# Kernel tuning notes

Hardware: AMD Instinct MI355X
Metric: run time of the kernel (lower is better)

Reference implementation:

```python
import jax, jax.numpy as jnp
import numpy as np

B, C, H, W, D = 512, 256, 6, 8, 8


def setup_inputs() -> dict:
    key = jax.random.key(0)
    k1, k2, k3 = jax.random.split(key, 3)
    x = jax.random.normal(k1, (B, C, H, W, D), dtype=jnp.float32)
    adj = jax.random.normal(k2, (C, C), dtype=jnp.float32)
    para = jax.random.normal(k3, (1, C, H, W, D), dtype=jnp.float32)
    return {"x": x, "adj": adj, "para": para}


def reference(x, adj, para):
    b, c, h, w, d = x.shape
    fea = x.reshape(b, c, h * w * d)              # (b, c, HWD)
    c_adj = x.mean(axis=(2, 3, 4))                # AdaptiveAvgPool3d(1) -> (b, c)
    # torch: t1 (1,c), t2 (c,1); (t1 - t2)[i, j] = c_adj[j] - c_adj[i]
    diff = c_adj[:, None, :] - c_adj[:, :, None]  # (b, c, c)
    s = jnp.abs(jnp.abs(jax.nn.sigmoid(diff) - 0.5) - 0.5) * 2.0
    s = (s + jnp.swapaxes(s, 1, 2)) * 0.5         # symmetrize
    # batched (adj * s) @ fea  -> (b, c, HWD)
    out = jnp.einsum('bij,bjk->bik', adj[None, :, :] * s, fea)
    out = out.reshape(b, c, h, w, d) * para       # broadcast (1,c,h,w,d)
    return jax.nn.relu(out)
```

## Files before the change

kernel.cpp:

```cpp
#include <hip/hip_runtime.h>

#define B_   512
#define C_   256
#define HWD_ 384

typedef __bf16 bf16x8 __attribute__((ext_vector_type(8)));
typedef float  f32x4  __attribute__((ext_vector_type(4)));

__global__ __launch_bounds__(256) void mean_kernel(const float* __restrict__ x,
                                                   float* __restrict__ cadj) {
    const int row  = (blockIdx.x << 2) + (threadIdx.x >> 6);
    const int lane = threadIdx.x & 63;
    const float2* p = (const float2*)(x + (size_t)row * HWD_);
    float s = 0.f;
#pragma unroll
    for (int t = 0; t < 3; ++t) {
        float2 v = p[lane + (t << 6)];
        s += v.x + v.y;
    }
#pragma unroll
    for (int off = 32; off; off >>= 1) s += __shfl_xor(s, off, 64);
    if (lane == 0) cadj[row] = s * (1.0f / HWD_);
}

__global__ __launch_bounds__(256) void gemm_kernel(const float* __restrict__ x,
                                                   const float* __restrict__ adj,
                                                   const float* __restrict__ para,
                                                   const float* __restrict__ cadj,
                                                   float* __restrict__ out) {
    const int mt = blockIdx.x;
    const int nt = blockIdx.y;
    const int b  = blockIdx.z;
    const int i0 = mt * 128;
    const int n0 = nt * 128;

    __shared__ __bf16 As[128][40];
    __shared__ __bf16 Bs[128][40];

    const int tid  = threadIdx.x;
    const int lane = tid & 63;
    const int w    = tid >> 6;
    const int wm   = w & 1, wn = w >> 1;
    const int lm   = lane & 15, quad = lane >> 4;

    const float* ca = cadj + b * C_;

    const int a_row  = tid >> 1;
    const int a_half = tid & 1;
    const float ca_i = ca[i0 + a_row];

    const int b_n  = tid & 127;
    const int b_jg = tid >> 7;

    f32x4 acc[4][4];
#pragma unroll
    for (int mm = 0; mm < 4; ++mm)
#pragma unroll
        for (int nn = 0; nn < 4; ++nn)
            acc[mm][nn] = (f32x4){0.f, 0.f, 0.f, 0.f};

    for (int k0 = 0; k0 < C_; k0 += 32) {
        __syncthreads();
        {
            const float* ap = adj + (size_t)(i0 + a_row) * C_ + k0 + a_half * 16;
            float4 av[4];
#pragma unroll
            for (int q = 0; q < 4; ++q) av[q] = ((const float4*)ap)[q];
            bf16x8 pk0, pk1;
#pragma unroll
            for (int jj = 0; jj < 16; ++jj) {
                float aval = ((const float*)av)[jj];
                float d = ca[k0 + a_half * 16 + jj] - ca_i;
                float t = __expf(-fabsf(d));
                float s = 2.f * t / (1.f + t);
                float v = aval * s;
                if (jj < 8) pk0[jj & 7] = (__bf16)v;
                else        pk1[jj & 7] = (__bf16)v;
            }
            *(bf16x8*)&As[a_row][a_half * 16]     = pk0;
            *(bf16x8*)&As[a_row][a_half * 16 + 8] = pk1;
        }
        {
            const float* xp = x + (size_t)(b * C_ + k0 + b_jg * 16) * HWD_ + n0 + b_n;
            bf16x8 pk0, pk1;
#pragma unroll
            for (int jj = 0; jj < 16; ++jj) {
                float v = xp[(size_t)jj * HWD_];
                if (jj < 8) pk0[jj & 7] = (__bf16)v;
                else        pk1[jj & 7] = (__bf16)v;
            }
            *(bf16x8*)&Bs[b_n][b_jg * 16]     = pk0;
            *(bf16x8*)&Bs[b_n][b_jg * 16 + 8] = pk1;
        }
        __syncthreads();
        bf16x8 af[4], bfr[4];
#pragma unroll
        for (int mm = 0; mm < 4; ++mm)
            af[mm] = *(const bf16x8*)&As[wm * 64 + mm * 16 + lm][quad * 8];
#pragma unroll
        for (int nn = 0; nn < 4; ++nn)
            bfr[nn] = *(const bf16x8*)&Bs[wn * 64 + nn * 16 + lm][quad * 8];
#pragma unroll
        for (int mm = 0; mm < 4; ++mm)
#pragma unroll
            for (int nn = 0; nn < 4; ++nn)
                acc[mm][nn] = __builtin_amdgcn_mfma_f32_16x16x32_bf16(
                    af[mm], bfr[nn], acc[mm][nn], 0, 0, 0);
    }

#pragma unroll
    for (int mm = 0; mm < 4; ++mm) {
#pragma unroll
        for (int r = 0; r < 4; ++r) {
            const int i = i0 + wm * 64 + mm * 16 + quad * 4 + r;
            const float* pp = para + (size_t)i * HWD_;
            float* op = out + ((size_t)b * C_ + i) * HWD_;
#pragma unroll
            for (int nn = 0; nn < 4; ++nn) {
                const int n = n0 + wn * 64 + nn * 16 + lm;
                float v = acc[mm][nn][r] * pp[n];
                op[n] = v > 0.f ? v : 0.f;
            }
        }
    }
}

extern "C" void kernel_launch(void* const* d_in, const int* in_sizes, int n_in,
                              void* d_out, int out_size, void* d_ws, size_t ws_size,
                              hipStream_t stream) {
    const float* x    = (const float*)d_in[0];
    const float* adj  = (const float*)d_in[1];
    const float* para = (const float*)d_in[2];
    float* out  = (float*)d_out;
    float* cadj = (float*)d_ws;

    mean_kernel<<<dim3((B_ * C_) / 4), 256, 0, stream>>>(x, cadj);
    gemm_kernel<<<dim3(2, 3, B_), 256, 0, stream>>>(x, adj, para, cadj, out);
}
```

Baseline: 432.6 us.

## Pre-pack A and B operands into MFMA fragment layout in workspace

Adds prep kernels: one converts x to bf16 in MFMA fragment order while also computing the channel means, and another builds the scaled adj*s matrix per batch in fragment order. The GEMM then loads fragments directly from global memory with no LDS staging or barriers. This avoids recomputing the similarity weights for every tile and makes the GEMM loads coalesced. In exchange it writes and re-reads roughly 150MB of bf16 workspace and needs a large workspace, falling back to the old path if the workspace is too small.

```diff
diff --git a/kernel.cpp b/kernel.cpp
--- a/kernel.cpp
+++ b/kernel.cpp
@@ -3,9 +3,152 @@
 #define B_   512
 #define C_   256
 #define HWD_ 384
+#define KC_  8
+#define IT_  16
+#define NT_  24
 
 typedef __bf16 bf16x8 __attribute__((ext_vector_type(8)));
 typedef float  f32x4  __attribute__((ext_vector_type(4)));
+
+#define CADJ_BYTES  ((size_t)B_ * C_ * 4)
+#define AFRAG_BYTES ((size_t)B_ * KC_ * IT_ * 1024)
+#define BFRAG_BYTES ((size_t)B_ * KC_ * NT_ * 1024)
+#define WS_NEEDED   (CADJ_BYTES + AFRAG_BYTES + BFRAG_BYTES)
+
+__global__ __launch_bounds__(256) void bprep_kernel(const float* __restrict__ x,
+                                                    float* __restrict__ cadj,
+                                                    bf16x8* __restrict__ bfrag) {
+    const int b = blockIdx.x, kc = blockIdx.y;
+    const int t = threadIdx.x, lane = t & 63, w = t >> 6;
+    const int quad = lane >> 4, lm = lane & 15;
+
+    const float* xb = x + ((size_t)b * C_ + kc * 32 + quad * 8) * HWD_ + lm;
+    bf16x8* dst = bfrag + ((size_t)(b * KC_ + kc) * NT_) * 64 + lane;
+
+    float acc[8];
+#pragma unroll
+    for (int j = 0; j < 8; ++j) acc[j] = 0.f;
+
+#pragma unroll
+    for (int ss = 0; ss < 6; ++ss) {
+        const int nt = w + 4 * ss;
+        const float* p = xb + nt * 16;
+        bf16x8 pk;
+#pragma unroll
+        for (int j = 0; j < 8; ++j) {
+            float v = p[(size_t)j * HWD_];
+            acc[j] += v;
+            pk[j] = (__bf16)v;
+        }
+        dst[(size_t)nt * 64] = pk;
+    }
+
+#pragma unroll
+    for (int m = 1; m < 16; m <<= 1)
+#pragma unroll
+        for (int j = 0; j < 8; ++j) acc[j] += __shfl_xor(acc[j], m, 64);
+
+    __shared__ float red[128];
+    if (lm == 0)
+#pragma unroll
+        for (int j = 0; j < 8; ++j) red[w * 32 + quad * 8 + j] = acc[j];
+    __syncthreads();
+    if (t < 32) {
+        float s = 0.f;
+#pragma unroll
+        for (int w2 = 0; w2 < 4; ++w2) s += red[w2 * 32 + t];
+        cadj[b * C_ + kc * 32 + t] = s * (1.0f / HWD_);
+    }
+}
+
+__global__ __launch_bounds__(256) void aprep_kernel(const float* __restrict__ adj,
+                                                    const float* __restrict__ cadj,
+                                                    bf16x8* __restrict__ afrag) {
+    const int b = blockIdx.x, kc = blockIdx.y;
+    const int t = threadIdx.x, lane = t & 63, wq = t >> 6;
+    const int quad = lane >> 4, lm = lane & 15;
+
+    __shared__ float sca[C_];
+    sca[t] = cadj[b * C_ + t];
+    __syncthreads();
+
+    const int kb = kc * 32 + quad * 8;
+    bf16x8* dst = afrag + ((size_t)(b * KC_ + kc) * IT_) * 64 + lane;
+
+#pragma unroll
+    for (int r = 0; r < 4; ++r) {
+        const int it = wq * 4 + r;
+        const int i  = it * 16 + lm;
+        const float4* ap = (const float4*)(adj + (size_t)i * C_ + kb);
+        float4 a0 = ap[0], a1 = ap[1];
+        const float ca_i = sca[i];
+        bf16x8 pk;
+#pragma unroll
+        for (int j = 0; j < 8; ++j) {
+            float av = (j < 4) ? (&a0.x)[j] : (&a1.x)[j - 4];
+            float d  = sca[kb + j] - ca_i;
+            float e  = __expf(-fabsf(d));
+            float s  = 2.f * e / (1.f + e);
+            pk[j] = (__bf16)(av * s);
+        }
+        dst[(size_t)it * 64] = pk;
+    }
+}
+
+__global__ __launch_bounds__(256) void gemm_kernel(const bf16x8* __restrict__ afrag,
+                                                   const bf16x8* __restrict__ bfrag,
+                                                   const float* __restrict__ para,
+                                                   float* __restrict__ out) {
+    const int mt = blockIdx.x;
+    const int nt = blockIdx.y;
+    const int b  = blockIdx.z;
+    const int i0 = mt * 128, n0 = nt * 128;
+
+    const int t = threadIdx.x, lane = t & 63, w = t >> 6;
+    const int wm = w & 1, wn = w >> 1;
+    const int lm = lane & 15, quad = lane >> 4;
+
+    const bf16x8* abase = afrag + (size_t)b * KC_ * IT_ * 64 + (size_t)(mt * 8 + wm * 4) * 64 + lane;
+    const bf16x8* bbase = bfrag + (size_t)b * KC_ * NT_ * 64 + (size_t)(nt * 8 + wn * 4) * 64 + lane;
+
+    f32x4 acc[4][4];
+#pragma unroll
+    for (int mm = 0; mm < 4; ++mm)
+#pragma unroll
+        for (int nn = 0; nn < 4; ++nn)
+            acc[mm][nn] = (f32x4){0.f, 0.f, 0.f, 0.f};
+
+#pragma unroll
+    for (int kc = 0; kc < KC_; ++kc) {
+        bf16x8 af[4], bfr[4];
+#pragma unroll
+        for (int mm = 0; mm < 4; ++mm) af[mm] = abase[(size_t)(kc * IT_ + mm) * 64];
+#pragma unroll
+        for (int nn = 0; nn < 4; ++nn) bfr[nn] = bbase[(size_t)(kc * NT_ + nn) * 64];
+#pragma unroll
+        for (int mm = 0; mm < 4; ++mm)
+#pragma unroll
+            for (int nn = 0; nn < 4; ++nn)
+                acc[mm][nn] = __builtin_amdgcn_mfma_f32_16x16x32_bf16(
+                    af[mm], bfr[nn], acc[mm][nn], 0, 0, 0);
+    }
+
+#pragma unroll
+    for (int mm = 0; mm < 4; ++mm) {
+#pragma unroll
+        for (int r = 0; r < 4; ++r) {
+            const int i = i0 + wm * 64 + mm * 16 + quad * 4 + r;
+            const float* pp = para + (size_t)i * HWD_;
+            float* op = out + ((size_t)b * C_ + i) * HWD_;
+#pragma unroll
+            for (int nn = 0; nn < 4; ++nn) {
+                const int n = n0 + wn * 64 + nn * 16 + lm;
+                float v = acc[mm][nn][r] * pp[n];
+                op[n] = v > 0.f ? v : 0.f;
+            }
+        }
+    }
+}
 
 __global__ __launch_bounds__(256) void mean_kernel(const float* __restrict__ x,
                                                    float* __restrict__ cadj) {
@@ -14,8 +157,8 @@
     const float2* p = (const float2*)(x + (size_t)row * HWD_);
     float s = 0.f;
 #pragma unroll
-    for (int t = 0; t < 3; ++t) {
-        float2 v = p[lane + (t << 6)];
+    for (int tt = 0; tt < 3; ++tt) {
+        float2 v = p[lane + (tt << 6)];
         s += v.x + v.y;
     }
 #pragma unroll
@@ -23,42 +166,26 @@
     if (lane == 0) cadj[row] = s * (1.0f / HWD_);
 }
 
-__global__ __launch_bounds__(256) void gemm_kernel(const float* __restrict__ x,
-                                                   const float* __restrict__ adj,
-                                                   const float* __restrict__ para,
-                                                   const float* __restrict__ cadj,
-                                                   float* __restrict__ out) {
-    const int mt = blockIdx.x;
-    const int nt = blockIdx.y;
-    const int b  = blockIdx.z;
-    const int i0 = mt * 128;
-    const int n0 = nt * 128;
-
+__global__ __launch_bounds__(256) void gemm_fb(const float* __restrict__ x,
+                                               const float* __restrict__ adj,
+                                               const float* __restrict__ para,
+                                               const float* __restrict__ cadj,
+                                               float* __restrict__ out) {
+    const int mt = blockIdx.x, nt = blockIdx.y, b = blockIdx.z;
+    const int i0 = mt * 128, n0 = nt * 128;
     __shared__ __bf16 As[128][40];
     __shared__ __bf16 Bs[128][40];
-
-    const int tid  = threadIdx.x;
-    const int lane = tid & 63;
-    const int w    = tid >> 6;
-    const int wm   = w & 1, wn = w >> 1;
-    const int lm   = lane & 15, quad = lane >> 4;
-
+    const int tid = threadIdx.x, lane = tid & 63, w = tid >> 6;
+    const int wm = w & 1, wn = w >> 1, lm = lane & 15, quad = lane >> 4;
     const float* ca = cadj + b * C_;
-
-    const int a_row  = tid >> 1;
-    const int a_half = tid & 1;
+    const int a_row = tid >> 1, a_half = tid & 1;
     const float ca_i = ca[i0 + a_row];
-
-    const int b_n  = tid & 127;
-    const int b_jg = tid >> 7;
-
+    const int b_n = tid & 127, b_jg = tid >> 7;
     f32x4 acc[4][4];
 #pragma unroll
     for (int mm = 0; mm < 4; ++mm)
 #pragma unroll
-        for (int nn = 0; nn < 4; ++nn)
-            acc[mm][nn] = (f32x4){0.f, 0.f, 0.f, 0.f};
-
+        for (int nn = 0; nn < 4; ++nn) acc[mm][nn] = (f32x4){0.f, 0.f, 0.f, 0.f};
     for (int k0 = 0; k0 < C_; k0 += 32) {
         __syncthreads();
         {
@@ -71,11 +198,10 @@
             for (int jj = 0; jj < 16; ++jj) {
                 float aval = ((const float*)av)[jj];
                 float d = ca[k0 + a_half * 16 + jj] - ca_i;
-                float t = __expf(-fabsf(d));
-                float s = 2.f * t / (1.f + t);
+                float tt = __expf(-fabsf(d));
+                float s = 2.f * tt / (1.f + tt);
                 float v = aval * s;
-                if (jj < 8) pk0[jj & 7] = (__bf16)v;
-                else        pk1[jj & 7] = (__bf16)v;
+                if (jj < 8) pk0[jj & 7] = (__bf16)v; else pk1[jj & 7] = (__bf16)v;
             }
             *(bf16x8*)&As[a_row][a_half * 16]     = pk0;
             *(bf16x8*)&As[a_row][a_half * 16 + 8] = pk1;
@@ -86,8 +212,7 @@
 #pragma unroll
             for (int jj = 0; jj < 16; ++jj) {
                 float v = xp[(size_t)jj * HWD_];
-                if (jj < 8) pk0[jj & 7] = (__bf16)v;
-                else        pk1[jj & 7] = (__bf16)v;
+                if (jj < 8) pk0[jj & 7] = (__bf16)v; else pk1[jj & 7] = (__bf16)v;
             }
             *(bf16x8*)&Bs[b_n][b_jg * 16]     = pk0;
             *(bf16x8*)&Bs[b_n][b_jg * 16 + 8] = pk1;
@@ -95,21 +220,17 @@
         __syncthreads();
         bf16x8 af[4], bfr[4];
 #pragma unroll
+        for (int mm = 0; mm < 4; ++mm) af[mm] = *(const bf16x8*)&As[wm * 64 + mm * 16 + lm][quad * 8];
+#pragma unroll
+        for (int nn = 0; nn < 4; ++nn) bfr[nn] = *(const bf16x8*)&Bs[wn * 64 + nn * 16 + lm][quad * 8];
+#pragma unroll
         for (int mm = 0; mm < 4; ++mm)
-            af[mm] = *(const bf16x8*)&As[wm * 64 + mm * 16 + lm][quad * 8];
-#pragma unroll
-        for (int nn = 0; nn < 4; ++nn)
-            bfr[nn] = *(const bf16x8*)&Bs[wn * 64 + nn * 16 + lm][quad * 8];
-#pragma unroll
-        for (int mm = 0; mm < 4; ++mm)
 #pragma unroll
             for (int nn = 0; nn < 4; ++nn)
-                acc[mm][nn] = __builtin_amdgcn_mfma_f32_16x16x32_bf16(
-                    af[mm], bfr[nn], acc[mm][nn], 0, 0, 0);
-    }
-
-#pragma unroll
-    for (int mm = 0; mm < 4; ++mm) {
+                acc[mm][nn] = __builtin_amdgcn_mfma_f32_16x16x32_bf16(af[mm], bfr[nn], acc[mm][nn], 0, 0, 0);
+    }
+#pragma unroll
+    for (int mm = 0; mm < 4; ++mm)
 #pragma unroll
         for (int r = 0; r < 4; ++r) {
             const int i = i0 + wm * 64 + mm * 16 + quad * 4 + r;
@@ -122,7 +243,6 @@
                 op[n] = v > 0.f ? v : 0.f;
             }
         }
-    }
 }
 
 extern "C" void kernel_launch(void* const* d_in, const int* in_sizes, int n_in,
@@ -131,9 +251,18 @@
     const float* x    = (const float*)d_in[0];
     const float* adj  = (const float*)d_in[1];
     const float* para = (const float*)d_in[2];
-    float* out  = (float*)d_out;
-    float* cadj = (float*)d_ws;
-
-    mean_kernel<<<dim3((B_ * C_) / 4), 256, 0, stream>>>(x, cadj);
-    gemm_kernel<<<dim3(2, 3, B_), 256, 0, stream>>>(x, adj, para, cadj, out);
-}
+    float* out = (float*)d_out;
+
+    if (ws_size >= WS_NEEDED) {
+        float*  cadj  = (float*)d_ws;
+        bf16x8* afrag = (bf16x8*)((char*)d_ws + CADJ_BYTES);
+        bf16x8* bfrag = (bf16x8*)((char*)d_ws + CADJ_BYTES + AFRAG_BYTES);
+        bprep_kernel<<<dim3(B_, KC_), 256, 0, stream>>>(x, cadj, bfrag);
+        aprep_kernel<<<dim3(B_, KC_), 256, 0, stream>>>(adj, cadj, afrag);
+        gemm_kernel<<<dim3(2, 3, B_), 256, 0, stream>>>(afrag, bfrag, para, out);
+    } else {
+        float* cadj = (float*)d_ws;
+        mean_kernel<<<dim3((B_ * C_) / 4), 256, 0, stream>>>(x, cadj);
+        gemm_fb<<<dim3(2, 3, B_), 256, 0, stream>>>(x, adj, para, cadj, out);
+    }
+}
```

Measured after the change: 470.6 us. 1.09x slower.

## Software-pipeline GEMM with register-prefetched x tiles and direct-from-global A fragments

Applied to the files above, without the earlier changes.

Restructures the GEMM main loop into a multi-stage pipeline. x tiles are fetched with coalesced float4 loads into registers two stages ahead, staged through a padded fp32 LDS buffer, then transposed into a bf16 fragment layout in a double-buffered LDS area. The adj*similarity A fragments are now computed straight from global memory into registers per wave, using cadj cached in LDS and a hardware reciprocal, instead of being built cooperatively in LDS. This drops the strided uncoalesced x loads and one barrier per iteration, at the cost of more LDS use, redundant A-side exp work across waves, and a launch-bounds occupancy hint.

```diff
diff --git a/kernel.cpp b/kernel.cpp
--- a/kernel.cpp
+++ b/kernel.cpp
@@ -3,6 +3,7 @@
 #define B_   512
 #define C_   256
 #define HWD_ 384
+#define TS   132
 
 typedef __bf16 bf16x8 __attribute__((ext_vector_type(8)));
 typedef float  f32x4  __attribute__((ext_vector_type(4)));
@@ -23,34 +24,32 @@
     if (lane == 0) cadj[row] = s * (1.0f / HWD_);
 }
 
-__global__ __launch_bounds__(256) void gemm_kernel(const float* __restrict__ x,
-                                                   const float* __restrict__ adj,
-                                                   const float* __restrict__ para,
-                                                   const float* __restrict__ cadj,
-                                                   float* __restrict__ out) {
+__global__ __launch_bounds__(256, 2) void gemm_kernel(const float* __restrict__ x,
+                                                      const float* __restrict__ adj,
+                                                      const float* __restrict__ para,
+                                                      const float* __restrict__ cadj,
+                                                      float* __restrict__ out) {
     const int mt = blockIdx.x;
     const int nt = blockIdx.y;
     const int b  = blockIdx.z;
-    const int i0 = mt * 128;
-    const int n0 = nt * 128;
+    const int i0 = mt * 128, n0 = nt * 128;
 
-    __shared__ __bf16 As[128][40];
-    __shared__ __bf16 Bs[128][40];
+    const int t = threadIdx.x, lane = t & 63, w = t >> 6;
+    const int wm = w & 1, wn = w >> 1;
+    const int lm = lane & 15, quad = lane >> 4;
 
-    const int tid  = threadIdx.x;
-    const int lane = tid & 63;
-    const int w    = tid >> 6;
-    const int wm   = w & 1, wn = w >> 1;
-    const int lm   = lane & 15, quad = lane >> 4;
+    __shared__ float  sca[C_];
+    __shared__ float  T32[2][32 * TS];
+    __shared__ __bf16 Bsf[2][8 * 64 * 8];
 
-    const float* ca = cadj + b * C_;
+    sca[t] = cadj[b * C_ + t];
 
-    const int a_row  = tid >> 1;
-    const int a_half = tid & 1;
-    const float ca_i = ca[i0 + a_row];
+    const int br = t >> 5;
+    const int bg = t & 31;
+    const float* xbase = x + (size_t)b * C_ * HWD_ + n0 + 4 * bg;
 
-    const int b_n  = tid & 127;
-    const int b_jg = tid >> 7;
+    const int s2c = t >> 5, s2h = (t >> 4) & 1, s2lm = t & 15;
+    const int s2n = s2c * 16 + s2lm;
 
     f32x4 acc[4][4];
 #pragma unroll
@@ -59,53 +58,77 @@
         for (int nn = 0; nn < 4; ++nn)
             acc[mm][nn] = (f32x4){0.f, 0.f, 0.f, 0.f};
 
-    for (int k0 = 0; k0 < C_; k0 += 32) {
-        __syncthreads();
-        {
-            const float* ap = adj + (size_t)(i0 + a_row) * C_ + k0 + a_half * 16;
-            float4 av[4];
+    float4 greg[4];
 #pragma unroll
-            for (int q = 0; q < 4; ++q) av[q] = ((const float4*)ap)[q];
-            bf16x8 pk0, pk1;
+    for (int p = 0; p < 4; ++p)
+        greg[p] = *(const float4*)(xbase + (size_t)(br + 8 * p) * HWD_);
 #pragma unroll
-            for (int jj = 0; jj < 16; ++jj) {
-                float aval = ((const float*)av)[jj];
-                float d = ca[k0 + a_half * 16 + jj] - ca_i;
-                float t = __expf(-fabsf(d));
-                float s = 2.f * t / (1.f + t);
-                float v = aval * s;
-                if (jj < 8) pk0[jj & 7] = (__bf16)v;
-                else        pk1[jj & 7] = (__bf16)v;
+    for (int p = 0; p < 4; ++p)
+        *(float4*)&T32[0][(br + 8 * p) * TS + 4 * bg] = greg[p];
+#pragma unroll
+    for (int p = 0; p < 4; ++p)
+        greg[p] = *(const float4*)(xbase + (size_t)(32 + br + 8 * p) * HWD_);
+    __syncthreads();
+
+    float ca_i[4];
+#pragma unroll
+    for (int mm = 0; mm < 4; ++mm) ca_i[mm] = sca[i0 + wm * 64 + mm * 16 + lm];
+
+#pragma unroll
+    for (int q = 0; q <= 8; ++q) {
+        if (q < 8) {
+            float v[16];
+#pragma unroll
+            for (int j2 = 0; j2 < 16; ++j2)
+                v[j2] = T32[q & 1][(s2h * 16 + j2) * TS + s2n];
+            bf16x8 p0, p1;
+#pragma unroll
+            for (int j = 0; j < 8; ++j) { p0[j] = (__bf16)v[j]; p1[j] = (__bf16)v[8 + j]; }
+            *(bf16x8*)&Bsf[q & 1][(s2c * 64 + (2 * s2h) * 16 + s2lm) * 8]     = p0;
+            *(bf16x8*)&Bsf[q & 1][(s2c * 64 + (2 * s2h + 1) * 16 + s2lm) * 8] = p1;
+        }
+        if (q + 1 < 8) {
+#pragma unroll
+            for (int p = 0; p < 4; ++p)
+                *(float4*)&T32[(q + 1) & 1][(br + 8 * p) * TS + 4 * bg] = greg[p];
+        }
+        if (q + 2 < 8) {
+#pragma unroll
+            for (int p = 0; p < 4; ++p)
+                greg[p] = *(const float4*)(xbase + (size_t)((q + 2) * 32 + br + 8 * p) * HWD_);
+        }
+        if (q >= 1) {
+            const int kc = q - 1;
+            f32x4 ck0 = *(const f32x4*)&sca[kc * 32 + quad * 8];
+            f32x4 ck1 = *(const f32x4*)&sca[kc * 32 + quad * 8 + 4];
+            bf16x8 af[4];
+#pragma unroll
+            for (int mm = 0; mm < 4; ++mm) {
+                const float* ap = adj + (size_t)(i0 + wm * 64 + mm * 16 + lm) * C_ + kc * 32 + quad * 8;
+                float4 a0 = *(const float4*)ap;
+                float4 a1 = *(const float4*)(ap + 4);
+#pragma unroll
+                for (int j = 0; j < 8; ++j) {
+                    float ck = (j < 4) ? ck0[j] : ck1[j - 4];
+                    float d  = ck - ca_i[mm];
+                    float e  = __expf(-fabsf(d));
+                    float s  = 2.f * e * __builtin_amdgcn_rcpf(1.f + e);
+                    float av = (j < 4) ? (&a0.x)[j] : (&a1.x)[j - 4];
+                    af[mm][j] = (__bf16)(av * s);
+                }
             }
-            *(bf16x8*)&As[a_row][a_half * 16]     = pk0;
-            *(bf16x8*)&As[a_row][a_half * 16 + 8] = pk1;
-        }
-        {
-            const float* xp = x + (size_t)(b * C_ + k0 + b_jg * 16) * HWD_ + n0 + b_n;
-            bf16x8 pk0, pk1;
-#pragma unroll
-            for (int jj = 0; jj < 16; ++jj) {
-                float v = xp[(size_t)jj * HWD_];
-                if (jj < 8) pk0[jj & 7] = (__bf16)v;
-                else        pk1[jj & 7] = (__bf16)v;
-            }
-            *(bf16x8*)&Bs[b_n][b_jg * 16]     = pk0;
-            *(bf16x8*)&Bs[b_n][b_jg * 16 + 8] = pk1;
-        }
-        __syncthreads();
-        bf16x8 af[4], bfr[4];
-#pragma unroll
-        for (int mm = 0; mm < 4; ++mm)
-            af[mm] = *(const bf16x8*)&As[wm * 64 + mm * 16 + lm][quad * 8];
-#pragma unroll
-        for (int nn = 0; nn < 4; ++nn)
-            bfr[nn] = *(const bf16x8*)&Bs[wn * 64 + nn * 16 + lm][quad * 8];
-#pragma unroll
-        for (int mm = 0; mm < 4; ++mm)
+            bf16x8 bfr[4];
 #pragma unroll
             for (int nn = 0; nn < 4; ++nn)
-                acc[mm][nn] = __builtin_amdgcn_mfma_f32_16x16x32_bf16(
-                    af[mm], bfr[nn], acc[mm][nn], 0, 0, 0);
+                bfr[nn] = *(const bf16x8*)&Bsf[kc & 1][((wn * 4 + nn) * 64 + lane) * 8];
+#pragma unroll
+            for (int mm = 0; mm < 4; ++mm)
+#pragma unroll
+                for (int nn = 0; nn < 4; ++nn)
+                    acc[mm][nn] = __builtin_amdgcn_mfma_f32_16x16x32_bf16(
+                        af[mm], bfr[nn], acc[mm][nn], 0, 0, 0);
+        }
+        if (q < 8) __syncthreads();
     }
 
 #pragma unroll
```

After: 511.6 us. 18.3% more time.
